# Performance work log

Hardware: AMD Instinct MI355X
Metric: run time of the kernel (lower is better)

Reference implementation:

```python
import jax, jax.numpy as jnp
import numpy as np

N = 50000      # nodes
E = 800000     # edges (before self loops)
G = 256        # graphs in batch
L = 3          # num_layers
H = 4          # heads
C = 32         # hidden_dim per head
D = 128        # input_dim == H*C
EMB = 128      # embed_dim


def setup_inputs() -> dict:
    key = jax.random.key(0)
    ks = jax.random.split(key, 9)
    x = jax.random.normal(ks[0], (N, D), dtype=jnp.float32)
    edge_index = jax.random.randint(ks[1], (2, E), 0, N, dtype=jnp.int32)
    batch = jnp.sort(jax.random.randint(ks[2], (N,), 0, G, dtype=jnp.int32))
    W = jax.random.normal(ks[3], (L, D, H * C), dtype=jnp.float32) / np.float32(np.sqrt(D))
    att_src = jax.random.normal(ks[4], (L, H, C), dtype=jnp.float32) * 0.1
    att_dst = jax.random.normal(ks[5], (L, H, C), dtype=jnp.float32) * 0.1
    bias = jnp.zeros((L, H * C), dtype=jnp.float32)
    ln_gamma = jnp.ones((L, H * C), dtype=jnp.float32)
    ln_beta = jnp.zeros((L, H * C), dtype=jnp.float32)
    W_out = jax.random.normal(ks[6], (2 * H * C, EMB), dtype=jnp.float32) / np.float32(np.sqrt(2 * H * C))
    b_out = jnp.zeros((EMB,), dtype=jnp.float32)
    return dict(x=x, edge_index=edge_index, batch=batch, W=W, att_src=att_src,
                att_dst=att_dst, bias=bias, ln_gamma=ln_gamma, ln_beta=ln_beta,
                W_out=W_out, b_out=b_out)


def _gat_layer(h_in, src, dst, W, a_src, a_dst, b):
    # PyG GATConv, concat=True, negative_slope=0.2, add_self_loops handled by caller
    h = (h_in @ W).reshape(N, H, C)                       # [N,H,C]
    al_s = jnp.einsum('nhc,hc->nh', h, a_src)             # [N,H]
    al_d = jnp.einsum('nhc,hc->nh', h, a_dst)             # [N,H]
    e = jax.nn.leaky_relu(al_s[src] + al_d[dst], 0.2)     # [Etot,H]
    m = jax.ops.segment_max(e, dst, num_segments=N)       # segment softmax over dst
    p = jnp.exp(e - m[dst])
    denom = jax.ops.segment_sum(p, dst, num_segments=N)
    alpha = p / denom[dst]                                # [Etot,H]
    agg = jax.ops.segment_sum(h[src] * alpha[..., None], dst, num_segments=N)
    return agg.reshape(N, H * C) + b


def _layer_norm(x, g, b, eps=1e-5):
    mu = x.mean(-1, keepdims=True)
    var = x.var(-1, keepdims=True)
    return (x - mu) * jax.lax.rsqrt(var + eps) * g + b


def reference(x, edge_index, batch, W, att_src, att_dst, bias, ln_gamma, ln_beta, W_out, b_out):
    loops = jnp.arange(N, dtype=edge_index.dtype)
    src = jnp.concatenate([edge_index[0], loops])         # add self loops (PyG default)
    dst = jnp.concatenate([edge_index[1], loops])
    out = x
    for l in range(L):
        out = _gat_layer(out, src, dst, W[l], att_src[l], att_dst[l], bias[l])
        out = _layer_norm(out, ln_gamma[l], ln_beta[l])
        out = jax.nn.leaky_relu(out, 0.1)
    gmax = jax.ops.segment_max(out, batch, num_segments=G)           # global_max_pool
    gsum = jax.ops.segment_sum(out, batch, num_segments=G)
    cnt = jax.ops.segment_sum(jnp.ones((N, 1), out.dtype), batch, num_segments=G)
    gmean = gsum / jnp.maximum(cnt, 1.0)                              # global_mean_pool
    pooled = jnp.concatenate([gmax, gmean], axis=1)                   # [G, 2*H*C]
    return pooled @ W_out + b_out
```

## Files before the change

### kernel.cpp

```cpp
#include <hip/hip_runtime.h>

#define NN 50000
#define EE 800000
#define ETOT (EE + NN)
#define GG 256
#define LL 3
#define HH 4
#define DD 128
#define NBLK ((NN + 255) / 256)
#define NXCD 8
#define DPX ((NN + NXCD - 1) / NXCD)
#define CSRB 1024

#define NEG_SENT (-1e30f)

__device__ __forceinline__ unsigned short f2bf(float x) {
  unsigned u = __float_as_uint(x);
  unsigned r = u + 0x7FFFu + ((u >> 16) & 1u);
  return (unsigned short)(r >> 16);
}

__global__ __launch_bounds__(256) void gemm_al_k(const float* __restrict__ A,
                                                 const float* __restrict__ Wl,
                                                 const float* __restrict__ asrc,
                                                 const float* __restrict__ adst,
                                                 unsigned short* __restrict__ Hb,
                                                 float* __restrict__ al_s,
                                                 float* __restrict__ al_d) {
  __shared__ float sW[128 * 128];
  __shared__ float sA[32][128];
  int tid = threadIdx.x;
#pragma unroll
  for (int j = 0; j < 16; ++j) {
    int idx = j * 256 + tid;
    *(float4*)&sW[idx * 4] = *(const float4*)&Wl[idx * 4];
  }
  int row0 = blockIdx.x * 32;
#pragma unroll
  for (int j = 0; j < 4; ++j) {
    int idx = j * 256 + tid;
    int r = idx >> 5, c4 = idx & 31;
    int gr = row0 + r;
    float4 v = (gr < NN) ? *(const float4*)&A[(size_t)gr * DD + c4 * 4]
                         : make_float4(0.f, 0.f, 0.f, 0.f);
    *(float4*)&sA[r][c4 * 4] = v;
  }
  __syncthreads();
  int tc = tid & 31;
  int tr = tid >> 5;
  float acc[4][4] = {};
  for (int k = 0; k < 128; ++k) {
    float4 w = *(const float4*)&sW[k * 128 + tc * 4];
    float a[4];
#pragma unroll
    for (int r = 0; r < 4; ++r) a[r] = sA[tr * 4 + r][k];
#pragma unroll
    for (int r = 0; r < 4; ++r) {
      acc[r][0] += a[r] * w.x;
      acc[r][1] += a[r] * w.y;
      acc[r][2] += a[r] * w.z;
      acc[r][3] += a[r] * w.w;
    }
  }
  float4 as4 = *(const float4*)&asrc[tc * 4];
  float4 ad4 = *(const float4*)&adst[tc * 4];
  int hg = tc >> 3;
  float ps[4], pd[4];
#pragma unroll
  for (int r = 0; r < 4; ++r) {
    ps[r] = acc[r][0] * as4.x + acc[r][1] * as4.y + acc[r][2] * as4.z + acc[r][3] * as4.w;
    pd[r] = acc[r][0] * ad4.x + acc[r][1] * ad4.y + acc[r][2] * ad4.z + acc[r][3] * ad4.w;
  }
#pragma unroll
  for (int off = 4; off; off >>= 1) {
#pragma unroll
    for (int r = 0; r < 4; ++r) {
      ps[r] += __shfl_xor(ps[r], off);
      pd[r] += __shfl_xor(pd[r], off);
    }
  }
#pragma unroll
  for (int r = 0; r < 4; ++r) {
    int gr = row0 + tr * 4 + r;
    if (gr < NN) {
      unsigned lo = (unsigned)f2bf(acc[r][0]) | ((unsigned)f2bf(acc[r][1]) << 16);
      unsigned hi = (unsigned)f2bf(acc[r][2]) | ((unsigned)f2bf(acc[r][3]) << 16);
      uint2 w = {lo, hi};
      *(uint2*)&Hb[(size_t)gr * DD + tc * 4] = w;
      if ((tc & 7) == 0) {
        al_s[gr * 4 + hg] = ps[r];
        al_d[gr * 4 + hg] = pd[r];
      }
    }
  }
}

__global__ __launch_bounds__(256) void deg_k(const int* __restrict__ ei,
                                             int* __restrict__ deg) {
  int lo = (blockIdx.x & 7) * DPX, hi = lo + DPX;
  int stride = (gridDim.x >> 3) * 256;
  for (int e = (blockIdx.x >> 3) * 256 + threadIdx.x; e < ETOT; e += stride) {
    int d = (e < EE) ? ei[EE + e] : (e - EE);
    if (d >= lo && d < hi) atomicAdd(&deg[d], 1);
  }
}

__global__ __launch_bounds__(256) void scanA_k(const int* __restrict__ deg,
                                               int* __restrict__ rp,
                                               int* __restrict__ bsum) {
  __shared__ int sb[256];
  int t = threadIdx.x, b = blockIdx.x, i = b * 256 + t;
  int d = (i < NN) ? deg[i] : 0;
  sb[t] = d;
  __syncthreads();
#pragma unroll
  for (int off = 1; off < 256; off <<= 1) {
    int v = (t >= off) ? sb[t - off] : 0;
    __syncthreads();
    sb[t] += v;
    __syncthreads();
  }
  if (i < NN) rp[i] = sb[t] - d;
  if (t == 255) bsum[b] = sb[255];
}

__global__ __launch_bounds__(256) void scanB_k(const int* __restrict__ bsum,
                                               int* __restrict__ boff) {
  __shared__ int sb[256];
  int t = threadIdx.x;
  int d = (t < NBLK) ? bsum[t] : 0;
  sb[t] = d;
  __syncthreads();
#pragma unroll
  for (int off = 1; off < 256; off <<= 1) {
    int v = (t >= off) ? sb[t - off] : 0;
    __syncthreads();
    sb[t] += v;
    __syncthreads();
  }
  if (t < NBLK) boff[t] = sb[t] - d;
}

__global__ __launch_bounds__(256) void scanC_k(int* __restrict__ rp,
                                               const int* __restrict__ boff,
                                               int* __restrict__ cur) {
  int b = blockIdx.x, i = b * 256 + threadIdx.x;
  if (i < NN) {
    int v = rp[i] + boff[b];
    rp[i] = v;
    cur[i] = v;
  }
  if (i == 0) rp[NN] = ETOT;
}

__global__ __launch_bounds__(256) void scatter_k(const int* __restrict__ ei,
                                                 int* __restrict__ cur,
                                                 int* __restrict__ col) {
  int lo = (blockIdx.x & 7) * DPX, hi = lo + DPX;
  int stride = (gridDim.x >> 3) * 256;
  for (int e = (blockIdx.x >> 3) * 256 + threadIdx.x; e < ETOT; e += stride) {
    int s, d;
    if (e < EE) { s = ei[e]; d = ei[EE + e]; }
    else        { s = e - EE; d = s; }
    if (d >= lo && d < hi) {
      int pos = atomicAdd(&cur[d], 1);
      col[pos] = s;
    }
  }
}

__global__ __launch_bounds__(64) void gstart_k(const int* __restrict__ batch,
                                               int* __restrict__ gs) {
  int g = blockIdx.x * 64 + threadIdx.x;
  if (g > GG) return;
  int lo = 0, hi = NN;
  while (lo < hi) {
    int mid = (lo + hi) >> 1;
    if (batch[mid] < g) lo = mid + 1; else hi = mid;
  }
  gs[g] = lo;
}

__global__ __launch_bounds__(256) void agg_k(const int* __restrict__ rp,
                                             const int* __restrict__ col,
                                             const float* __restrict__ als,
                                             const float* __restrict__ ald,
                                             const unsigned short* __restrict__ Hb,
                                             const float* __restrict__ bias,
                                             const float* __restrict__ gamma,
                                             const float* __restrict__ beta,
                                             float* __restrict__ outb) {
  __shared__ float salpha[4][4][65];
  __shared__ int   scol[4][64];
  int wave = threadIdx.x >> 6, lane = threadIdx.x & 63;
  int n = blockIdx.x * 4 + wave;
  if (n >= NN) return;
  int e0 = rp[n], e1 = rp[n + 1];
  int deg = e1 - e0;
  float4 ad = *(const float4*)&ald[(size_t)n * 4];
  int hh = lane >> 4;
  float a0 = 0.f, a1 = 0.f;

  if (deg <= 64) {
    int sn = (lane < deg) ? col[e0 + lane] : -1;
    float4 as;
    if (sn >= 0) as = *(const float4*)&als[(size_t)sn * 4];
    else         as = make_float4(0.f, 0.f, 0.f, 0.f);
    float vv[4] = {as.x + ad.x, as.y + ad.y, as.z + ad.z, as.w + ad.w};
#pragma unroll
    for (int h = 0; h < 4; ++h) {
      float t = vv[h];
      t = t > 0.f ? t : 0.2f * t;
      vv[h] = (sn >= 0) ? t : NEG_SENT;
    }
    float m[4] = {vv[0], vv[1], vv[2], vv[3]};
#pragma unroll
    for (int off = 32; off; off >>= 1) {
#pragma unroll
      for (int h = 0; h < 4; ++h) m[h] = fmaxf(m[h], __shfl_xor(m[h], off));
    }
    float p[4], s[4];
#pragma unroll
    for (int h = 0; h < 4; ++h) {
      p[h] = (sn >= 0) ? __expf(vv[h] - m[h]) : 0.f;
      s[h] = p[h];
    }
#pragma unroll
    for (int off = 32; off; off >>= 1) {
#pragma unroll
      for (int h = 0; h < 4; ++h) s[h] += __shfl_xor(s[h], off);
    }
    scol[wave][lane] = sn;
#pragma unroll
    for (int h = 0; h < 4; ++h)
      salpha[wave][h][lane] = __fdividef(p[h], s[h]);
    asm volatile("s_waitcnt lgkmcnt(0)" ::: "memory");
#pragma unroll 4
    for (int j = 0; j < deg; ++j) {
      int snj = scol[wave][j];
      float alpha = salpha[wave][hh][j];
      unsigned pck = *(const unsigned*)&Hb[(size_t)snj * DD + 2 * lane];
      float h0 = __uint_as_float(pck << 16);
      float h1 = __uint_as_float(pck & 0xFFFF0000u);
      a0 = __fmaf_rn(alpha, h0, a0);
      a1 = __fmaf_rn(alpha, h1, a1);
    }
  } else {
    float m[4] = {NEG_SENT, NEG_SENT, NEG_SENT, NEG_SENT};
    float s[4] = {0.f, 0.f, 0.f, 0.f};
    for (int e = e0 + lane; e < e1; e += 64) {
      int sn = col[e];
      float4 as = *(const float4*)&als[(size_t)sn * 4];
      float v[4] = {as.x + ad.x, as.y + ad.y, as.z + ad.z, as.w + ad.w};
#pragma unroll
      for (int h = 0; h < 4; ++h) {
        float vvv = v[h] > 0.f ? v[h] : 0.2f * v[h];
        if (vvv > m[h]) { s[h] = s[h] * __expf(m[h] - vvv) + 1.f; m[h] = vvv; }
        else             s[h] += __expf(vvv - m[h]);
      }
    }
#pragma unroll
    for (int off = 32; off; off >>= 1) {
#pragma unroll
      for (int h = 0; h < 4; ++h) {
        float mo = __shfl_xor(m[h], off);
        float so = __shfl_xor(s[h], off);
        float M = fmaxf(m[h], mo);
        s[h] = s[h] * __expf(m[h] - M) + so * __expf(mo - M);
        m[h] = M;
      }
    }
    float mh = m[hh];
    float rdh = __fdividef(1.f, s[hh]);
    float adh = (hh == 0) ? ad.x : (hh == 1) ? ad.y : (hh == 2) ? ad.z : ad.w;
    int e = e0;
    while (e < e1) {
      int cnt = min(64, e1 - e);
      int myS = (lane < cnt) ? col[e + lane] : 0;
      for (int j = 0; j < cnt; ++j) {
        int sn = __shfl(myS, j);
        float v = als[(size_t)sn * 4 + hh] + adh;
        v = v > 0.f ? v : 0.2f * v;
        float alpha = __expf(v - mh) * rdh;
        unsigned pck = *(const unsigned*)&Hb[(size_t)sn * DD + 2 * lane];
        float h0 = __uint_as_float(pck << 16);
        float h1 = __uint_as_float(pck & 0xFFFF0000u);
        a0 = __fmaf_rn(alpha, h0, a0);
        a1 = __fmaf_rn(alpha, h1, a1);
      }
      e += cnt;
    }
  }

  int f0 = 2 * lane, f1 = 2 * lane + 1;
  float x0 = a0 + bias[f0], x1 = a1 + bias[f1];
  float sum = x0 + x1, ssq = x0 * x0 + x1 * x1;
#pragma unroll
  for (int off = 32; off; off >>= 1) {
    sum += __shfl_xor(sum, off);
    ssq += __shfl_xor(ssq, off);
  }
  float mu = sum * (1.f / 128.f);
  float var = ssq * (1.f / 128.f) - mu * mu;
  float rstd = rsqrtf(var + 1e-5f);
  float y0 = (x0 - mu) * rstd * gamma[f0] + beta[f0];
  float y1 = (x1 - mu) * rstd * gamma[f1] + beta[f1];
  y0 = y0 > 0.f ? y0 : 0.1f * y0;
  y1 = y1 > 0.f ? y1 : 0.1f * y1;
  float2 o = {y0, y1};
  *(float2*)&outb[(size_t)n * DD + f0] = o;
}

__global__ __launch_bounds__(128) void poolout_k(const float* __restrict__ xin,
                                                 const int* __restrict__ gs,
                                                 const float* __restrict__ Wout,
                                                 const float* __restrict__ bout,
                                                 float* __restrict__ out) {
  __shared__ float sp[256];
  int g = blockIdx.x, t = threadIdx.x;
  int n0 = gs[g], n1 = gs[g + 1];
  float mx = NEG_SENT, sm = 0.f;
#pragma unroll 4
  for (int n = n0; n < n1; ++n) {
    float v = xin[(size_t)n * DD + t];
    mx = fmaxf(mx, v);
    sm += v;
  }
  float c = (float)(n1 - n0);
  sp[t] = mx;
  sp[128 + t] = sm / fmaxf(c, 1.f);
  __syncthreads();
  float acc = bout[t];
#pragma unroll 8
  for (int k = 0; k < 256; ++k) acc = __fmaf_rn(sp[k], Wout[k * 128 + t], acc);
  out[(size_t)g * 128 + t] = acc;
}

extern "C" void kernel_launch(void* const* d_in, const int* in_sizes, int n_in,
                              void* d_out, int out_size, void* d_ws, size_t ws_size,
                              hipStream_t stream) {
  const float* x       = (const float*)d_in[0];
  const int*   ei      = (const int*)d_in[1];
  const int*   batch   = (const int*)d_in[2];
  const float* W       = (const float*)d_in[3];
  const float* att_src = (const float*)d_in[4];
  const float* att_dst = (const float*)d_in[5];
  const float* bias    = (const float*)d_in[6];
  const float* gamma   = (const float*)d_in[7];
  const float* beta    = (const float*)d_in[8];
  const float* Wout    = (const float*)d_in[9];
  const float* bout    = (const float*)d_in[10];
  float* out = (float*)d_out;

  char* ws = (char*)d_ws;
  unsigned short* Hb = (unsigned short*)ws; ws += (size_t)NN * DD * 2;
  float* AB   = (float*)ws; ws += (size_t)NN * DD * 4;
  float* als  = (float*)ws; ws += (size_t)NN * HH * 4;
  float* ald  = (float*)ws; ws += (size_t)NN * HH * 4;
  int*   rp   = (int*)ws;   ws += (size_t)(NN + 1) * 4;
  int*   deg  = (int*)ws;   ws += (size_t)NN * 4;
  int*   col  = (int*)ws;   ws += (size_t)ETOT * 4;
  int*   gs   = (int*)ws;   ws += (size_t)(GG + 1) * 4;
  int*   bsum = (int*)ws;   ws += (size_t)NBLK * 4;
  int*   boff = (int*)ws;   ws += (size_t)NBLK * 4;

  hipMemsetAsync(deg, 0, (size_t)NN * 4, stream);
  deg_k<<<CSRB, 256, 0, stream>>>(ei, deg);
  scanA_k<<<NBLK, 256, 0, stream>>>(deg, rp, bsum);
  scanB_k<<<1, 256, 0, stream>>>(bsum, boff);
  scanC_k<<<NBLK, 256, 0, stream>>>(rp, boff, deg);
  scatter_k<<<CSRB, 256, 0, stream>>>(ei, deg, col);
  gstart_k<<<(GG + 1 + 63) / 64, 64, 0, stream>>>(batch, gs);

  const float* in = x;
  for (int l = 0; l < LL; ++l) {
    gemm_al_k<<<(NN + 31) / 32, 256, 0, stream>>>(in, W + (size_t)l * DD * DD,
                                                  att_src + l * DD, att_dst + l * DD,
                                                  Hb, als, ald);
    agg_k<<<(NN + 3) / 4, 256, 0, stream>>>(rp, col, als, ald, Hb,
                                            bias + l * DD, gamma + l * DD, beta + l * DD, AB);
    in = AB;
  }

  poolout_k<<<GG, 128, 0, stream>>>(AB, gs, Wout, bout, out);
}
```

Baseline: 360.4 us.

## Replace FP32 SIMT GEMM with split-bf16 MFMA and store activations as bf16 pairs

Replaces the scalar FP32 shared-memory GEMM with a bf16 MFMA GEMM that uses a hi/lo split (three MFMAs per tile) to recover near-FP32 accuracy. Weights are pre-split and transposed once by a new kernel. The aggregation kernel now writes its activations as hi/lo bf16 halves, which the next GEMM reads directly and pooling recombines. The aim is to cut the GEMM's compute cost. In exchange it adds three times the MFMA work, W fragments loaded straight from global memory with no LDS reuse, scattered 2-byte Hb stores, and a small accuracy loss.

```diff
diff --git a/kernel.cpp b/kernel.cpp
--- a/kernel.cpp
+++ b/kernel.cpp
@@ -11,85 +11,124 @@
 #define NXCD 8
 #define DPX ((NN + NXCD - 1) / NXCD)
 #define CSRB 1024
+#define GB ((NN + 63) / 64)
 
 #define NEG_SENT (-1e30f)
+
+typedef __attribute__((ext_vector_type(8))) short s16x8;
+typedef __attribute__((ext_vector_type(4))) float f32x4;
+union U4 { uint4 u; s16x8 s; };
 
 __device__ __forceinline__ unsigned short f2bf(float x) {
   unsigned u = __float_as_uint(x);
   unsigned r = u + 0x7FFFu + ((u >> 16) & 1u);
   return (unsigned short)(r >> 16);
 }
-
-__global__ __launch_bounds__(256) void gemm_al_k(const float* __restrict__ A,
-                                                 const float* __restrict__ Wl,
-                                                 const float* __restrict__ asrc,
-                                                 const float* __restrict__ adst,
-                                                 unsigned short* __restrict__ Hb,
-                                                 float* __restrict__ al_s,
-                                                 float* __restrict__ al_d) {
-  __shared__ float sW[128 * 128];
-  __shared__ float sA[32][128];
-  int tid = threadIdx.x;
-#pragma unroll
-  for (int j = 0; j < 16; ++j) {
-    int idx = j * 256 + tid;
-    *(float4*)&sW[idx * 4] = *(const float4*)&Wl[idx * 4];
-  }
-  int row0 = blockIdx.x * 32;
-#pragma unroll
-  for (int j = 0; j < 4; ++j) {
-    int idx = j * 256 + tid;
-    int r = idx >> 5, c4 = idx & 31;
-    int gr = row0 + r;
-    float4 v = (gr < NN) ? *(const float4*)&A[(size_t)gr * DD + c4 * 4]
-                         : make_float4(0.f, 0.f, 0.f, 0.f);
-    *(float4*)&sA[r][c4 * 4] = v;
-  }
-  __syncthreads();
-  int tc = tid & 31;
-  int tr = tid >> 5;
-  float acc[4][4] = {};
-  for (int k = 0; k < 128; ++k) {
-    float4 w = *(const float4*)&sW[k * 128 + tc * 4];
-    float a[4];
-#pragma unroll
-    for (int r = 0; r < 4; ++r) a[r] = sA[tr * 4 + r][k];
+__device__ __forceinline__ float bf2f(unsigned short b) {
+  return __uint_as_float((unsigned)b << 16);
+}
+
+__global__ __launch_bounds__(256) void wsplit_k(const float* __restrict__ W,
+                                                unsigned short* __restrict__ Wth,
+                                                unsigned short* __restrict__ Wtl) {
+  int i = blockIdx.x * 256 + threadIdx.x;
+  if (i >= LL * DD * DD) return;
+  int l = i / (DD * DD), rem = i % (DD * DD);
+  int n = rem >> 7, k = rem & 127;
+  float w = W[(size_t)l * DD * DD + k * DD + n];
+  unsigned short hb = f2bf(w);
+  Wth[i] = hb;
+  Wtl[i] = f2bf(w - bf2f(hb));
+}
+
+template <int L0>
+__global__ __launch_bounds__(256) void gemm_mfma_k(const float* __restrict__ Ax,
+                                                   const unsigned short* __restrict__ Ahi,
+                                                   const unsigned short* __restrict__ Alo,
+                                                   const unsigned short* __restrict__ Wth,
+                                                   const unsigned short* __restrict__ Wtl,
+                                                   const float* __restrict__ asrc,
+                                                   const float* __restrict__ adst,
+                                                   unsigned short* __restrict__ Hb,
+                                                   float* __restrict__ al_s,
+                                                   float* __restrict__ al_d) {
+  int wid = threadIdx.x >> 6, lane = threadIdx.x & 63;
+  int r0 = blockIdx.x * 64 + wid * 16;
+  int c0 = lane & 15, kg = lane >> 4;
+  int row = r0 + c0;
+  int rl = row < NN ? row : NN - 1;
+  f32x4 acc[8];
+#pragma unroll
+  for (int nt = 0; nt < 8; ++nt) acc[nt] = (f32x4){0.f, 0.f, 0.f, 0.f};
+
+#pragma unroll
+  for (int ks = 0; ks < 4; ++ks) {
+    s16x8 ah, al;
+    if (L0) {
+      const float* ap = &Ax[(size_t)rl * DD + ks * 32 + kg * 8];
+      float4 v0 = *(const float4*)ap;
+      float4 v1 = *(const float4*)(ap + 4);
+      float av[8] = {v0.x, v0.y, v0.z, v0.w, v1.x, v1.y, v1.z, v1.w};
+#pragma unroll
+      for (int e = 0; e < 8; ++e) {
+        unsigned short hb = f2bf(av[e]);
+        ah[e] = (short)hb;
+        al[e] = (short)f2bf(av[e] - bf2f(hb));
+      }
+    } else {
+      U4 uh, ul;
+      uh.u = *(const uint4*)&Ahi[(size_t)rl * DD + ks * 32 + kg * 8];
+      ul.u = *(const uint4*)&Alo[(size_t)rl * DD + ks * 32 + kg * 8];
+      ah = uh.s;
+      al = ul.s;
+    }
+#pragma unroll
+    for (int nt = 0; nt < 8; ++nt) {
+      int wrow = nt * 16 + c0;
+      U4 wh, wl;
+      wh.u = *(const uint4*)&Wth[(size_t)wrow * DD + ks * 32 + kg * 8];
+      wl.u = *(const uint4*)&Wtl[(size_t)wrow * DD + ks * 32 + kg * 8];
+      acc[nt] = __builtin_amdgcn_mfma_f32_16x16x32_bf16(ah, wh.s, acc[nt], 0, 0, 0);
+      acc[nt] = __builtin_amdgcn_mfma_f32_16x16x32_bf16(al, wh.s, acc[nt], 0, 0, 0);
+      acc[nt] = __builtin_amdgcn_mfma_f32_16x16x32_bf16(ah, wl.s, acc[nt], 0, 0, 0);
+    }
+  }
+
+  float ps[4][4] = {}, pd[4][4] = {};
+#pragma unroll
+  for (int nt = 0; nt < 8; ++nt) {
+    int col = nt * 16 + c0;
+    float sv = asrc[col], dv = adst[col];
+    int hg = nt >> 1;
 #pragma unroll
     for (int r = 0; r < 4; ++r) {
-      acc[r][0] += a[r] * w.x;
-      acc[r][1] += a[r] * w.y;
-      acc[r][2] += a[r] * w.z;
-      acc[r][3] += a[r] * w.w;
-    }
-  }
-  float4 as4 = *(const float4*)&asrc[tc * 4];
-  float4 ad4 = *(const float4*)&adst[tc * 4];
-  int hg = tc >> 3;
-  float ps[4], pd[4];
+      ps[hg][r] += acc[nt][r] * sv;
+      pd[hg][r] += acc[nt][r] * dv;
+    }
+  }
+#pragma unroll
+  for (int off = 1; off < 16; off <<= 1) {
+#pragma unroll
+    for (int h = 0; h < 4; ++h)
+#pragma unroll
+      for (int r = 0; r < 4; ++r) {
+        ps[h][r] += __shfl_xor(ps[h][r], off);
+        pd[h][r] += __shfl_xor(pd[h][r], off);
+      }
+  }
 #pragma unroll
   for (int r = 0; r < 4; ++r) {
-    ps[r] = acc[r][0] * as4.x + acc[r][1] * as4.y + acc[r][2] * as4.z + acc[r][3] * as4.w;
-    pd[r] = acc[r][0] * ad4.x + acc[r][1] * ad4.y + acc[r][2] * ad4.z + acc[r][3] * ad4.w;
-  }
-#pragma unroll
-  for (int off = 4; off; off >>= 1) {
-#pragma unroll
-    for (int r = 0; r < 4; ++r) {
-      ps[r] += __shfl_xor(ps[r], off);
-      pd[r] += __shfl_xor(pd[r], off);
-    }
-  }
-#pragma unroll
-  for (int r = 0; r < 4; ++r) {
-    int gr = row0 + tr * 4 + r;
-    if (gr < NN) {
-      unsigned lo = (unsigned)f2bf(acc[r][0]) | ((unsigned)f2bf(acc[r][1]) << 16);
-      unsigned hi = (unsigned)f2bf(acc[r][2]) | ((unsigned)f2bf(acc[r][3]) << 16);
-      uint2 w = {lo, hi};
-      *(uint2*)&Hb[(size_t)gr * DD + tc * 4] = w;
-      if ((tc & 7) == 0) {
-        al_s[gr * 4 + hg] = ps[r];
-        al_d[gr * 4 + hg] = pd[r];
+    int grr = r0 + kg * 4 + r;
+    if (grr < NN) {
+#pragma unroll
+      for (int nt = 0; nt < 8; ++nt)
+        Hb[(size_t)grr * DD + nt * 16 + c0] = f2bf(acc[nt][r]);
+      if (c0 == 0) {
+#pragma unroll
+        for (int h = 0; h < 4; ++h) {
+          al_s[grr * 4 + h] = ps[h][r];
+          al_d[grr * 4 + h] = pd[h][r];
+        }
       }
     }
   }
@@ -189,7 +228,8 @@
                                              const float* __restrict__ bias,
                                              const float* __restrict__ gamma,
                                              const float* __restrict__ beta,
-                                             float* __restrict__ outb) {
+                                             unsigned short* __restrict__ ABh,
+                                             unsigned short* __restrict__ ABl) {
   __shared__ float salpha[4][4][65];
   __shared__ int   scol[4][64];
   int wave = threadIdx.x >> 6, lane = threadIdx.x & 63;
@@ -307,11 +347,14 @@
   float y1 = (x1 - mu) * rstd * gamma[f1] + beta[f1];
   y0 = y0 > 0.f ? y0 : 0.1f * y0;
   y1 = y1 > 0.f ? y1 : 0.1f * y1;
-  float2 o = {y0, y1};
-  *(float2*)&outb[(size_t)n * DD + f0] = o;
-}
-
-__global__ __launch_bounds__(128) void poolout_k(const float* __restrict__ xin,
+  unsigned short h0b = f2bf(y0), h1b = f2bf(y1);
+  unsigned short l0b = f2bf(y0 - bf2f(h0b)), l1b = f2bf(y1 - bf2f(h1b));
+  *(unsigned*)&ABh[(size_t)n * DD + f0] = (unsigned)h0b | ((unsigned)h1b << 16);
+  *(unsigned*)&ABl[(size_t)n * DD + f0] = (unsigned)l0b | ((unsigned)l1b << 16);
+}
+
+__global__ __launch_bounds__(128) void poolout_k(const unsigned short* __restrict__ ABh,
+                                                 const unsigned short* __restrict__ ABl,
                                                  const int* __restrict__ gs,
                                                  const float* __restrict__ Wout,
                                                  const float* __restrict__ bout,
@@ -322,7 +365,7 @@
   float mx = NEG_SENT, sm = 0.f;
 #pragma unroll 4
   for (int n = n0; n < n1; ++n) {
-    float v = xin[(size_t)n * DD + t];
+    float v = bf2f(ABh[(size_t)n * DD + t]) + bf2f(ABl[(size_t)n * DD + t]);
     mx = fmaxf(mx, v);
     sm += v;
   }
@@ -353,8 +396,11 @@
   float* out = (float*)d_out;
 
   char* ws = (char*)d_ws;
-  unsigned short* Hb = (unsigned short*)ws; ws += (size_t)NN * DD * 2;
-  float* AB   = (float*)ws; ws += (size_t)NN * DD * 4;
+  unsigned short* Hb  = (unsigned short*)ws; ws += (size_t)NN * DD * 2;
+  unsigned short* ABh = (unsigned short*)ws; ws += (size_t)NN * DD * 2;
+  unsigned short* ABl = (unsigned short*)ws; ws += (size_t)NN * DD * 2;
+  unsigned short* Wth = (unsigned short*)ws; ws += (size_t)LL * DD * DD * 2;
+  unsigned short* Wtl = (unsigned short*)ws; ws += (size_t)LL * DD * DD * 2;
   float* als  = (float*)ws; ws += (size_t)NN * HH * 4;
   float* ald  = (float*)ws; ws += (size_t)NN * HH * 4;
   int*   rp   = (int*)ws;   ws += (size_t)(NN + 1) * 4;
@@ -371,16 +417,23 @@
   scanC_k<<<NBLK, 256, 0, stream>>>(rp, boff, deg);
   scatter_k<<<CSRB, 256, 0, stream>>>(ei, deg, col);
   gstart_k<<<(GG + 1 + 63) / 64, 64, 0, stream>>>(batch, gs);
-
-  const float* in = x;
+  wsplit_k<<<(LL * DD * DD + 255) / 256, 256, 0, stream>>>(W, Wth, Wtl);
+
   for (int l = 0; l < LL; ++l) {
-    gemm_al_k<<<(NN + 31) / 32, 256, 0, stream>>>(in, W + (size_t)l * DD * DD,
-                                                  att_src + l * DD, att_dst + l * DD,
-                                                  Hb, als, ald);
+    const unsigned short* Wh = Wth + (size_t)l * DD * DD;
+    const unsigned short* Wl = Wtl + (size_t)l * DD * DD;
+    if (l == 0)
+      gemm_mfma_k<1><<<GB, 256, 0, stream>>>(x, ABh, ABl, Wh, Wl,
+                                             att_src + l * DD, att_dst + l * DD,
+                                             Hb, als, ald);
+    else
+      gemm_mfma_k<0><<<GB, 256, 0, stream>>>(x, ABh, ABl, Wh, Wl,
+                                             att_src + l * DD, att_dst + l * DD,
+                                             Hb, als, ald);
     agg_k<<<(NN + 3) / 4, 256, 0, stream>>>(rp, col, als, ald, Hb,
-                                            bias + l * DD, gamma + l * DD, beta + l * DD, AB);
-    in = AB;
-  }
-
-  poolout_k<<<GG, 128, 0, stream>>>(AB, gs, Wout, bout, out);
-}
+                                            bias + l * DD, gamma + l * DD, beta + l * DD,
+                                            ABh, ABl);
+  }
+
+  poolout_k<<<GG, 128, 0, stream>>>(ABh, ABl, gs, Wout, bout, out);
+}
```

Measured after the change: 382.1 us. +6.0%, slower.

## Split aggregation wave into two half-waves over edges; parallelize pooling across two halves

Applied to the files above, without the earlier changes.

In the low-degree aggregation path, each wave is split into two 32-lane halves that process alternating edges, each lane loading 8 bytes (4 bf16 features). The partial sums are combined with a cross-half shuffle before LayerNorm. This halves the serial edge-loop length and widens the loads, at the cost of an extra reduction and redundant LayerNorm work in the upper half. The pooling kernel now uses 256 threads, splitting both the node range and the output matmul K dimension across two halves joined through shared memory.

```diff
diff --git a/kernel.cpp b/kernel.cpp
--- a/kernel.cpp
+++ b/kernel.cpp
@@ -198,8 +198,6 @@
   int e0 = rp[n], e1 = rp[n + 1];
   int deg = e1 - e0;
   float4 ad = *(const float4*)&ald[(size_t)n * 4];
-  int hh = lane >> 4;
-  float a0 = 0.f, a1 = 0.f;
 
   if (deg <= 64) {
     int sn = (lane < deg) ? col[e0 + lane] : -1;
@@ -235,17 +233,55 @@
     for (int h = 0; h < 4; ++h)
       salpha[wave][h][lane] = __fdividef(p[h], s[h]);
     asm volatile("s_waitcnt lgkmcnt(0)" ::: "memory");
+
+    int sub = lane >> 5, fl = lane & 31;
+    int hh2 = fl >> 3;
+    float b0 = 0.f, b1 = 0.f, b2 = 0.f, b3 = 0.f;
 #pragma unroll 4
-    for (int j = 0; j < deg; ++j) {
+    for (int j = sub; j < deg; j += 2) {
       int snj = scol[wave][j];
-      float alpha = salpha[wave][hh][j];
-      unsigned pck = *(const unsigned*)&Hb[(size_t)snj * DD + 2 * lane];
-      float h0 = __uint_as_float(pck << 16);
-      float h1 = __uint_as_float(pck & 0xFFFF0000u);
-      a0 = __fmaf_rn(alpha, h0, a0);
-      a1 = __fmaf_rn(alpha, h1, a1);
+      float alpha = salpha[wave][hh2][j];
+      uint2 pck = *(const uint2*)&Hb[(size_t)snj * DD + fl * 4];
+      b0 = __fmaf_rn(alpha, __uint_as_float(pck.x << 16), b0);
+      b1 = __fmaf_rn(alpha, __uint_as_float(pck.x & 0xFFFF0000u), b1);
+      b2 = __fmaf_rn(alpha, __uint_as_float(pck.y << 16), b2);
+      b3 = __fmaf_rn(alpha, __uint_as_float(pck.y & 0xFFFF0000u), b3);
+    }
+    b0 += __shfl_xor(b0, 32);
+    b1 += __shfl_xor(b1, 32);
+    b2 += __shfl_xor(b2, 32);
+    b3 += __shfl_xor(b3, 32);
+
+    int f4 = fl * 4;
+    float4 bi = *(const float4*)&bias[f4];
+    float x0 = b0 + bi.x, x1 = b1 + bi.y, x2 = b2 + bi.z, x3 = b3 + bi.w;
+    float sum = x0 + x1 + x2 + x3;
+    float ssq = x0 * x0 + x1 * x1 + x2 * x2 + x3 * x3;
+#pragma unroll
+    for (int off = 16; off; off >>= 1) {
+      sum += __shfl_xor(sum, off);
+      ssq += __shfl_xor(ssq, off);
+    }
+    float mu = sum * (1.f / 128.f);
+    float var = ssq * (1.f / 128.f) - mu * mu;
+    float rstd = rsqrtf(var + 1e-5f);
+    float4 ga = *(const float4*)&gamma[f4];
+    float4 be = *(const float4*)&beta[f4];
+    float y0 = (x0 - mu) * rstd * ga.x + be.x;
+    float y1 = (x1 - mu) * rstd * ga.y + be.y;
+    float y2 = (x2 - mu) * rstd * ga.z + be.z;
+    float y3 = (x3 - mu) * rstd * ga.w + be.w;
+    y0 = y0 > 0.f ? y0 : 0.1f * y0;
+    y1 = y1 > 0.f ? y1 : 0.1f * y1;
+    y2 = y2 > 0.f ? y2 : 0.1f * y2;
+    y3 = y3 > 0.f ? y3 : 0.1f * y3;
+    if (sub == 0) {
+      float4 o = {y0, y1, y2, y3};
+      *(float4*)&outb[(size_t)n * DD + f4] = o;
     }
   } else {
+    int hh = lane >> 4;
+    float a0 = 0.f, a1 = 0.f;
     float m[4] = {NEG_SENT, NEG_SENT, NEG_SENT, NEG_SENT};
     float s[4] = {0.f, 0.f, 0.f, 0.f};
     for (int e = e0 + lane; e < e1; e += 64) {
@@ -290,50 +326,61 @@
       }
       e += cnt;
     }
-  }
-
-  int f0 = 2 * lane, f1 = 2 * lane + 1;
-  float x0 = a0 + bias[f0], x1 = a1 + bias[f1];
-  float sum = x0 + x1, ssq = x0 * x0 + x1 * x1;
-#pragma unroll
-  for (int off = 32; off; off >>= 1) {
-    sum += __shfl_xor(sum, off);
-    ssq += __shfl_xor(ssq, off);
-  }
-  float mu = sum * (1.f / 128.f);
-  float var = ssq * (1.f / 128.f) - mu * mu;
-  float rstd = rsqrtf(var + 1e-5f);
-  float y0 = (x0 - mu) * rstd * gamma[f0] + beta[f0];
-  float y1 = (x1 - mu) * rstd * gamma[f1] + beta[f1];
-  y0 = y0 > 0.f ? y0 : 0.1f * y0;
-  y1 = y1 > 0.f ? y1 : 0.1f * y1;
-  float2 o = {y0, y1};
-  *(float2*)&outb[(size_t)n * DD + f0] = o;
-}
-
-__global__ __launch_bounds__(128) void poolout_k(const float* __restrict__ xin,
+    int f0 = 2 * lane, f1 = 2 * lane + 1;
+    float x0 = a0 + bias[f0], x1 = a1 + bias[f1];
+    float sum = x0 + x1, ssq = x0 * x0 + x1 * x1;
+#pragma unroll
+    for (int off = 32; off; off >>= 1) {
+      sum += __shfl_xor(sum, off);
+      ssq += __shfl_xor(ssq, off);
+    }
+    float mu = sum * (1.f / 128.f);
+    float var = ssq * (1.f / 128.f) - mu * mu;
+    float rstd = rsqrtf(var + 1e-5f);
+    float y0 = (x0 - mu) * rstd * gamma[f0] + beta[f0];
+    float y1 = (x1 - mu) * rstd * gamma[f1] + beta[f1];
+    y0 = y0 > 0.f ? y0 : 0.1f * y0;
+    y1 = y1 > 0.f ? y1 : 0.1f * y1;
+    float2 o = {y0, y1};
+    *(float2*)&outb[(size_t)n * DD + f0] = o;
+  }
+}
+
+__global__ __launch_bounds__(256) void poolout_k(const float* __restrict__ xin,
                                                  const int* __restrict__ gs,
                                                  const float* __restrict__ Wout,
                                                  const float* __restrict__ bout,
                                                  float* __restrict__ out) {
   __shared__ float sp[256];
+  __shared__ float r0[256], r1[256];
   int g = blockIdx.x, t = threadIdx.x;
+  int f = t & 127, half = t >> 7;
   int n0 = gs[g], n1 = gs[g + 1];
+  int cnt = n1 - n0;
+  int mid = n0 + (cnt >> 1);
+  int a = half ? mid : n0;
+  int b = half ? n1 : mid;
   float mx = NEG_SENT, sm = 0.f;
-#pragma unroll 4
-  for (int n = n0; n < n1; ++n) {
-    float v = xin[(size_t)n * DD + t];
+  for (int n = a; n < b; ++n) {
+    float v = xin[(size_t)n * DD + f];
     mx = fmaxf(mx, v);
     sm += v;
   }
-  float c = (float)(n1 - n0);
-  sp[t] = mx;
-  sp[128 + t] = sm / fmaxf(c, 1.f);
-  __syncthreads();
-  float acc = bout[t];
+  r0[t] = mx;
+  r1[t] = sm;
+  __syncthreads();
+  if (t < 128) {
+    sp[t] = fmaxf(r0[t], r0[t + 128]);
+    sp[128 + t] = (r1[t] + r1[t + 128]) / fmaxf((float)cnt, 1.f);
+  }
+  __syncthreads();
+  float acc = half ? 0.f : bout[f];
+  int k0 = half * 128;
 #pragma unroll 8
-  for (int k = 0; k < 256; ++k) acc = __fmaf_rn(sp[k], Wout[k * 128 + t], acc);
-  out[(size_t)g * 128 + t] = acc;
+  for (int k = k0; k < k0 + 128; ++k) acc = __fmaf_rn(sp[k], Wout[k * 128 + f], acc);
+  r0[t] = acc;
+  __syncthreads();
+  if (t < 128) out[(size_t)g * 128 + f] = r0[t] + r0[t + 128];
 }
 
 extern "C" void kernel_launch(void* const* d_in, const int* in_sizes, int n_in,
@@ -382,5 +429,5 @@
     in = AB;
   }
 
-  poolout_k<<<GG, 128, 0, stream>>>(AB, gs, Wout, bout, out);
-}
+  poolout_k<<<GG, 256, 0, stream>>>(AB, gs, Wout, bout, out);
+}
```

Result: slower. 370.0 us (+2.7%).
